# Kernel tuning notes

Measured on AMD Instinct MI355X. Metric: run time of the kernel, lower is better.

The kernel has to match this reference:

```python
import jax, jax.numpy as jnp
import numpy as np

C = 96        # dim
HEADS = 8     # FrameHistoryRouter heads (StateAlignBlock forces heads=1)
WS = 4        # window_size = 2*scale_patchsize
NFC = 1       # num_frames_tocache
TOPK = 5
LOCAL_N = 4


def conv(x, w, stride=1, pad=0, groups=1):
    return jax.lax.conv_general_dilated(
        x, w, (stride, stride), [(pad, pad), (pad, pad)],
        dimension_numbers=("NCHW", "OIHW", "NCHW"), feature_group_count=groups)


def l2norm(x, axis):
    n = jnp.linalg.norm(x, axis=axis, keepdims=True)
    return x / jnp.maximum(n, 1e-12)


def setup_inputs() -> dict:
    key = jax.random.key(0)
    ks = jax.random.split(key, 16)
    def rn(i, shp, s=0.02):
        return jax.random.normal(ks[i], shp, dtype=jnp.float32) * s
    return {
        "x": jax.random.normal(ks[0], (2, C, 256, 256), dtype=jnp.float32),
        "sab_qk_w": rn(1, (2 * C, C, 1, 1)),
        "sab_qk_dw": rn(2, (2 * C, 1, 3, 3)),
        "sab_v_w": rn(3, (C, C, 1, 1)),
        "sab_v_dw": rn(4, (C, 1, 3, 3)),
        "sab_k2_w": rn(5, (2 * C, C, 1, 1)),
        "sab_k2_dw": rn(6, (2 * C, 1, WS, WS)),
        "sab_q2_w": rn(7, (2 * C, C, 1, 1)),
        "sab_q2_dw": rn(8, (2 * C, 1, WS, WS)),
        "sab_proj_w": rn(9, (C, C, 1, 1)),
        "sab_temp": jnp.ones((1, 1, 1), jnp.float32),
        "fhr_qkv_w": rn(10, (3 * C, C, 1, 1)),
        "fhr_qkv_dw": rn(11, (3 * C, 1, 3, 3)),
        "fhr_proj_w": rn(12, (C, C, 1, 1)),
        "fhr_temp": jnp.ones((HEADS, 1, 1), jnp.float32),
    }


def _forward(x, sab_qk_w, sab_qk_dw, sab_v_w, sab_v_dw, sab_k2_w, sab_k2_dw,
             sab_q2_w, sab_q2_dw, sab_proj_w, sab_temp,
             fhr_qkv_w, fhr_qkv_dw, fhr_proj_w, fhr_temp):
    b, c, h, w = x.shape
    # ---------- StateAlignBlock (no cache: first frame) ----------
    qk = conv(conv(x, sab_qk_w), sab_qk_dw, pad=1, groups=2 * c)
    q, k = jnp.split(qk, 2, axis=1)
    v = conv(conv(x, sab_v_w), sab_v_dw, pad=1, groups=c)
    k = conv(conv(k, sab_k2_w), sab_k2_dw, stride=WS, pad=1, groups=2 * c)
    q = conv(conv(q, sab_q2_w), sab_q2_dw, stride=WS, pad=1, groups=2 * c)
    H, W = q.shape[2], q.shape[3]            # = h//WS, w//WS
    N = H * W
    # b (1 d) h w -> b 1 1 (h w) d   with d = 2c
    q = q.reshape(b, 2 * c, N).transpose(0, 2, 1)[:, None, None]
    k = k.reshape(b, 2 * c, N).transpose(0, 2, 1)[:, None, None]
    # v: b (1 d) (p1 h) (p2 w) -> b 1 1 (h w) (p1 p2 d), p1=p2=WS, d=c
    h2, w2 = h // WS, w // WS
    v = v.reshape(b, c, WS, h2, WS, w2).transpose(0, 3, 5, 2, 4, 1)
    v = v.reshape(b, 1, 1, h2 * w2, WS * WS * c)
    q = l2norm(q, -1)
    k = l2norm(k, -1)
    attn = jnp.einsum("bfgnd,bfgmd->bfgnm", q, k) * sab_temp  # [b,1,1,N,N]
    # zero_out_non_top_k (top-5 along last dim; threshold form, ties negligible)
    kth = jax.lax.top_k(attn, TOPK)[0][..., TOPK - 1:TOPK]
    topk_mask = (attn >= kth).astype(attn.dtype)
    # local attention mask: manhattan distance <= LOCAL_N on the HxW patch grid
    yy, xx = jnp.meshgrid(jnp.arange(H), jnp.arange(W), indexing="ij")
    coords = jnp.stack([yy.ravel(), xx.ravel()], axis=-1)          # [N,2]
    dist = jnp.abs(coords[:, None, :] - coords[None, :, :]).sum(-1)
    local = (dist <= LOCAL_N).astype(attn.dtype)                   # [N,N]
    attn = attn * topk_mask + attn * local                         # as in torch
    # clipped_softmax
    zero = attn == 0
    s = jax.nn.softmax(jnp.where(zero, -jnp.inf, attn), axis=-1)
    s = jnp.where(zero, 0.0, s)
    s = s / s.sum(-1, keepdims=True)
    out = jnp.einsum("bfgnm,bfgmd->bfgnd", s, v)  # [b,1,1,N, WS*WS*c]
    F = 1  # curr_num_frames (no cache)
    # b f 1 (h w) (p1 p2 d) -> (b f) d (p1 h) (p2 w)
    out = out.reshape(b * F, h2, w2, WS, WS, c).transpose(0, 5, 3, 1, 4, 2)
    out = out.reshape(b * F, c, h, w)
    out = conv(out, sab_proj_w)
    aligned = out.reshape(b, F, c, h, w)
    k_s = k[:, -NFC:]  # [b,1,1,N,2c]
    v_s = v[:, -NFC:]
    # ---------- FrameHistoryRouter on aligned current frame ----------
    x2 = aligned[:, -1]
    qkv = conv(conv(x2, fhr_qkv_w), fhr_qkv_dw, pad=1, groups=3 * c)
    q2, k2, v2 = jnp.split(qkv, 3, axis=1)
    hd = c // HEADS
    q2 = q2.reshape(b, HEADS, hd, h * w)
    k2 = k2.reshape(b, HEADS, hd, h * w)
    v2 = v2.reshape(b, HEADS, hd, h * w)
    q2 = l2norm(q2, -1)
    k2 = l2norm(k2, -1)
    a2 = jnp.einsum("bhcn,bhdn->bhcd", q2, k2) * fhr_temp  # [b,H,hd,hd]
    a2 = jax.nn.softmax(a2, axis=-1)
    o2 = jnp.einsum("bhcd,bhdn->bhcn", a2, v2).reshape(b, c, h, w)
    o2 = conv(o2, fhr_proj_w)
    keep = int(NFC * c / HEADS)  # = hd
    return o2, k_s, v_s, k2[:, :, -keep:, :], v2[:, :, -keep:, :]


def reference(x, sab_qk_w, sab_qk_dw, sab_v_w, sab_v_dw, sab_k2_w, sab_k2_dw,
              sab_q2_w, sab_q2_dw, sab_proj_w, sab_temp,
              fhr_qkv_w, fhr_qkv_dw, fhr_proj_w, fhr_temp):
    return _forward(x, sab_qk_w, sab_qk_dw, sab_v_w, sab_v_dw, sab_k2_w,
                    sab_k2_dw, sab_q2_w, sab_q2_dw, sab_proj_w, sab_temp,
                    fhr_qkv_w, fhr_qkv_dw, fhr_proj_w, fhr_temp)
```

## Files before the change

kernel.cpp:

```cpp
#include <hip/hip_runtime.h>
#include <hip/hip_bf16.h>
#include <math.h>

#define HW 65536L

typedef __attribute__((ext_vector_type(8))) short bf16x8;
typedef __attribute__((ext_vector_type(4))) float f32x4;

__device__ __forceinline__ int iabs_(int v) { return v < 0 ? -v : v; }

__device__ __forceinline__ void rtn_split(float f, unsigned short* h, unsigned short* l) {
  __hip_bfloat16 hb = __float2bfloat16(f);
  float hf = __bfloat162float(hb);
  __hip_bfloat16 lb = __float2bfloat16(f - hf);
  *h = *(unsigned short*)&hb;
  *l = *(unsigned short*)&lb;
}

__global__ __launch_bounds__(256) void wsplit(
    const float* __restrict__ qk, const float* __restrict__ v,
    const float* __restrict__ q2, const float* __restrict__ k2,
    unsigned short* __restrict__ whl)
{
  const int e = blockIdx.x*256 + threadIdx.x;
  if (e >= 64512) return;
  const int row = e / 96, col = e - row*96;
  float f;
  if      (row <  192) f = qk[e];
  else if (row <  288) f = v [(row-192)*96+col];
  else if (row <  480) f = q2[(row-288)*96+col];
  else                 f = k2[(row-480)*96+col];
  rtn_split(f, &whl[e], &whl[110592 + e]);
}

__global__ __launch_bounds__(256) void wcomp1(
    const float* __restrict__ fq, const float* __restrict__ pj,
    unsigned short* __restrict__ whl)
{
  const int e = blockIdx.x*256 + threadIdx.x;
  if (e >= 27648) return;
  const int row = e / 96, col = e - row*96;
  float s = 0.f;
  #pragma unroll 8
  for (int c = 0; c < 96; c++) s = fmaf(fq[row*96 + c], pj[c*96 + col], s);
  rtn_split(s, &whl[(768+row)*96 + col], &whl[110592 + (768+row)*96 + col]);
}

__global__ __launch_bounds__(256) void wcomp2(
    const float* __restrict__ fp, const float* __restrict__ a2s,
    unsigned short* __restrict__ w2)
{
  const int e = blockIdx.x*256 + threadIdx.x;
  const int b = blockIdx.y;
  if (e >= 9216) return;
  const int co = e / 96, dg = e - co*96;
  const int h = dg / 12, d = dg - h*12;
  const float* ab = a2s + (((long)b*8 + h)*12)*12 + d;
  const float* fpb = fp + co*96 + h*12;
  float s = 0.f;
  #pragma unroll
  for (int c = 0; c < 12; c++) s = fmaf(fpb[c], ab[c*12], s);
  rtn_split(s, &w2[(long)b*9216 + e], &w2[18432 + (long)b*9216 + e]);
}

#define BLDS 104
__global__ __launch_bounds__(256) void conv1x1_mfma(
    const float* __restrict__ in, long in_bstride,
    const unsigned short* __restrict__ whl_hi, const unsigned short* __restrict__ whl_lo,
    long wbstride, int wrow0,
    float* __restrict__ out, long out_bstride,
    float* __restrict__ out2, long out2_bstride,
    float* __restrict__ out3, long out3_bstride,
    int ms1, int ms2, int mtiles, int mode)
{
  __shared__ unsigned short bhs[128*BLDS];
  __shared__ unsigned short bls[128*BLDS];
  const int t = threadIdx.x;
  const int p0 = blockIdx.x * 128;
  const int b = blockIdx.y;
  if (mode == 0) {
    #pragma unroll
    for (int it = 0; it < 6; it++) {
      const int idx = it*256 + t;
      const int g8 = idx >> 7;
      const int pix = idx & 127;
      const float* src = in + (long)b*in_bstride + (long)(g8*8)*HW + p0 + pix;
      unsigned hh[8], ll[8];
      #pragma unroll
      for (int j = 0; j < 8; j++) {
        float f = src[(long)j*HW];
        unsigned u = __float_as_uint(f);
        hh[j] = u >> 16;
        float lof = f - __uint_as_float(u & 0xFFFF0000u);
        __hip_bfloat16 lb = __float2bfloat16(lof);
        ll[j] = *(unsigned short*)&lb;
      }
      uint4 hv, lv;
      hv.x = hh[0]|(hh[1]<<16); hv.y = hh[2]|(hh[3]<<16);
      hv.z = hh[4]|(hh[5]<<16); hv.w = hh[6]|(hh[7]<<16);
      lv.x = ll[0]|(ll[1]<<16); lv.y = ll[2]|(ll[3]<<16);
      lv.z = ll[4]|(ll[5]<<16); lv.w = ll[6]|(ll[7]<<16);
      *(uint4*)(bhs + pix*BLDS + g8*8) = hv;
      *(uint4*)(bls + pix*BLDS + g8*8) = lv;
    }
  } else {
    const int pp = t >> 1, half = (t & 1)*48;
    const int p = p0 + pp;
    const int py = p >> 8, px = p & 255;
    const float* src = in + (long)b*in_bstride
        + ((long)((py & 63)*64 + (px & 63))*16 + ((py >> 6)*4 + (px >> 6)))*96 + half;
    #pragma unroll
    for (int j4 = 0; j4 < 12; j4++) {
      float4 v4 = *(const float4*)&src[j4*4];
      float fv[4] = {v4.x, v4.y, v4.z, v4.w};
      unsigned hh[4], ll[4];
      #pragma unroll
      for (int u4 = 0; u4 < 4; u4++) {
        unsigned u = __float_as_uint(fv[u4]);
        hh[u4] = u >> 16;
        float lof = fv[u4] - __uint_as_float(u & 0xFFFF0000u);
        __hip_bfloat16 lb = __float2bfloat16(lof);
        ll[u4] = *(unsigned short*)&lb;
      }
      uint2 hv, lv;
      hv.x = hh[0] | (hh[1] << 16); hv.y = hh[2] | (hh[3] << 16);
      lv.x = ll[0] | (ll[1] << 16); lv.y = ll[2] | (ll[3] << 16);
      *(uint2*)(bhs + pp*BLDS + half + j4*4) = hv;
      *(uint2*)(bls + pp*BLDS + half + j4*4) = lv;
    }
  }
  __syncthreads();
  const int lane = t & 63, w = t >> 6;
  const int fr = lane & 15, fk = lane >> 4;
  bf16x8 Bh[2][3], Bl[2][3];
  #pragma unroll
  for (int nt = 0; nt < 2; nt++)
    #pragma unroll
    for (int kt = 0; kt < 3; kt++) {
      const int pix = w*32 + nt*16 + fr;
      Bh[nt][kt] = *(const bf16x8*)(bhs + pix*BLDS + kt*32 + fk*8);
      Bl[nt][kt] = *(const bf16x8*)(bls + pix*BLDS + kt*32 + fk*8);
    }
  const long wb = (long)b*wbstride;
  for (int m = 0; m < mtiles; m++) {
    const long wbase = wb + (long)(wrow0 + m*16 + fr)*96 + fk*8;
    bf16x8 Ah[3], Al[3];
    #pragma unroll
    for (int kt = 0; kt < 3; kt++) {
      Ah[kt] = *(const bf16x8*)(whl_hi + wbase + kt*32);
      Al[kt] = *(const bf16x8*)(whl_lo + wbase + kt*32);
    }
    f32x4 acc[2] = {};
    #pragma unroll
    for (int nt = 0; nt < 2; nt++)
      #pragma unroll
      for (int kt = 0; kt < 3; kt++) {
        acc[nt] = __builtin_amdgcn_mfma_f32_16x16x32_bf16(Ah[kt], Bh[nt][kt], acc[nt], 0, 0, 0);
        acc[nt] = __builtin_amdgcn_mfma_f32_16x16x32_bf16(Ah[kt], Bl[nt][kt], acc[nt], 0, 0, 0);
        acc[nt] = __builtin_amdgcn_mfma_f32_16x16x32_bf16(Al[kt], Bh[nt][kt], acc[nt], 0, 0, 0);
      }
    int mo; float* dst;
    if (m < ms1)      { mo = m;       dst = out  + (long)b*out_bstride; }
    else if (m < ms2) { mo = m - ms1; dst = out2 + (long)b*out2_bstride; }
    else              { mo = m - ms2; dst = out3 + (long)b*out3_bstride; }
    dst += p0 + w*32;
    #pragma unroll
    for (int nt = 0; nt < 2; nt++)
      #pragma unroll
      for (int r = 0; r < 4; r++)
        dst[(long)(mo*16 + fk*4 + r)*HW + nt*16 + fr] = acc[nt][r];
  }
}

__global__ __launch_bounds__(256) void dw3x3v(
    const float* __restrict__ in, int inCH, const float* __restrict__ w,
    float* __restrict__ out, int outCH)
{
  const int t = threadIdx.x;
  const int p4 = blockIdx.x * 256 + t;
  const int ch = blockIdx.y, b = blockIdx.z;
  const int y = p4 >> 6, x0 = (p4 & 63) << 2;
  const float* ip = in + ((long)b*inCH + ch) * HW;
  const float* wp = w + ch*9;
  float a0 = 0.f, a1 = 0.f, a2 = 0.f, a3 = 0.f;
  #pragma unroll
  for (int dy = -1; dy <= 1; dy++) {
    const int yy = y + dy;
    if (yy < 0 || yy > 255) continue;
    const float* rp = ip + yy*256;
    const float4 c = *(const float4*)&rp[x0];
    const float left  = (x0 > 0)   ? rp[x0-1] : 0.f;
    const float right = (x0 < 252) ? rp[x0+4] : 0.f;
    const float w0 = wp[(dy+1)*3+0], w1 = wp[(dy+1)*3+1], w2 = wp[(dy+1)*3+2];
    a0 = fmaf(left, w0, a0); a0 = fmaf(c.x, w1, a0); a0 = fmaf(c.y, w2, a0);
    a1 = fmaf(c.x,  w0, a1); a1 = fmaf(c.y, w1, a1); a1 = fmaf(c.z, w2, a1);
    a2 = fmaf(c.y,  w0, a2); a2 = fmaf(c.z, w1, a2); a2 = fmaf(c.w, w2, a2);
    a3 = fmaf(c.z,  w0, a3); a3 = fmaf(c.w, w1, a3); a3 = fmaf(right, w2, a3);
  }
  float4 o; o.x = a0; o.y = a1; o.z = a2; o.w = a3;
  *(float4*)&out[((long)b*outCH + ch)*HW + y*256 + x0] = o;
}

__global__ __launch_bounds__(256) void dw3x3_vs(
    const float* __restrict__ in, const float* __restrict__ w,
    float* __restrict__ vs)
{
  __shared__ float tile[96*65];
  const int t = threadIdx.x;
  const int gb = blockIdx.x;
  const int b = blockIdx.y;
  const int y = gb >> 2, xb = gb & 3;
  #pragma unroll
  for (int i = 0; i < 6; i++) {
    const int idx = i*256 + t;
    const int ci = idx >> 4, q = idx & 15;
    const int x0 = xb*64 + q*4;
    const float* ip = in + ((long)b*96 + ci) * HW;
    const float* wp = w + ci*9;
    float a0 = 0.f, a1 = 0.f, a2 = 0.f, a3 = 0.f;
    #pragma unroll
    for (int dy = -1; dy <= 1; dy++) {
      const int yy = y + dy;
      if (yy < 0 || yy > 255) continue;
      const float* rp = ip + yy*256;
      const float4 c = *(const float4*)&rp[x0];
      const float left  = (x0 > 0)   ? rp[x0-1] : 0.f;
      const float right = (x0 < 252) ? rp[x0+4] : 0.f;
      const float w0 = wp[(dy+1)*3+0], w1 = wp[(dy+1)*3+1], w2 = wp[(dy+1)*3+2];
      a0 = fmaf(left, w0, a0); a0 = fmaf(c.x, w1, a0); a0 = fmaf(c.y, w2, a0);
      a1 = fmaf(c.x,  w0, a1); a1 = fmaf(c.y, w1, a1); a1 = fmaf(c.z, w2, a1);
      a2 = fmaf(c.y,  w0, a2); a2 = fmaf(c.z, w1, a2); a2 = fmaf(c.w, w2, a2);
      a3 = fmaf(c.z,  w0, a3); a3 = fmaf(c.w, w1, a3); a3 = fmaf(right, w2, a3);
    }
    const int xl = q*4;
    tile[ci*65 + xl    ] = a0;
    tile[ci*65 + xl + 1] = a1;
    tile[ci*65 + xl + 2] = a2;
    tile[ci*65 + xl + 3] = a3;
  }
  __syncthreads();
  const int blk = (y >> 6)*4 + xb;
  float* obase = vs + ((long)b*4096 + (long)(y & 63)*64) * 1536 + blk*96;
  #pragma unroll
  for (int i = 0; i < 24; i++) {
    const int idx = i*256 + t;
    const int nl = idx / 96, ci = idx % 96;
    obase[(long)nl*1536 + ci] = tile[ci*65 + nl];
  }
}

__global__ __launch_bounds__(256) void dw4x4s4v(
    const float* __restrict__ in, const float* __restrict__ w,
    float* __restrict__ out)
{
  const int t = threadIdx.x;
  const int p = blockIdx.x*256 + t;
  const int ch = blockIdx.y, b = blockIdx.z;
  const int oy = p >> 4, qx = p & 15;
  const int x0 = qx*16;
  const float* ip = in + (long)(b*192 + ch) * HW;
  const float* wp = w + ch*16;
  float a0 = 0.f, a1 = 0.f, a2 = 0.f, a3 = 0.f;
  #pragma unroll
  for (int ty = 0; ty < 4; ty++) {
    const int iy = 4*oy + ty - 1;
    if (iy < 0 || iy > 255) continue;
    const float* rp = ip + iy*256;
    float r[17];
    r[0] = (x0 > 0) ? rp[x0-1] : 0.f;
    #pragma unroll
    for (int k = 0; k < 4; k++) {
      float4 v4 = *(const float4*)&rp[x0 + k*4];
      r[1+k*4+0]=v4.x; r[1+k*4+1]=v4.y; r[1+k*4+2]=v4.z; r[1+k*4+3]=v4.w;
    }
    const float w0=wp[ty*4+0], w1=wp[ty*4+1], w2=wp[ty*4+2], w3=wp[ty*4+3];
    a0=fmaf(r[ 0],w0,a0); a0=fmaf(r[ 1],w1,a0); a0=fmaf(r[ 2],w2,a0); a0=fmaf(r[ 3],w3,a0);
    a1=fmaf(r[ 4],w0,a1); a1=fmaf(r[ 5],w1,a1); a1=fmaf(r[ 6],w2,a1); a1=fmaf(r[ 7],w3,a1);
    a2=fmaf(r[ 8],w0,a2); a2=fmaf(r[ 9],w1,a2); a2=fmaf(r[10],w2,a2); a2=fmaf(r[11],w3,a2);
    a3=fmaf(r[12],w0,a3); a3=fmaf(r[13],w1,a3); a3=fmaf(r[14],w2,a3); a3=fmaf(r[15],w3,a3);
  }
  float4 o; o.x=a0; o.y=a1; o.z=a2; o.w=a3;
  *(float4*)&out[(long)(b*192 + ch)*4096 + oy*64 + qx*4] = o;
}

__global__ __launch_bounds__(256) void l2n192(
    const float* __restrict__ inA, float* __restrict__ outA,
    const float* __restrict__ inB, float* __restrict__ outB)
{
  const int t = threadIdx.x;
  const int wid = t >> 6, lane = t & 63;
  const int gw2 = blockIdx.x * 4 + wid;
  const int sel = gw2 >> 13;
  const int gw = gw2 & 8191;
  const int b = gw >> 12, n = gw & 4095;
  const float* ip = (sel ? inB : inA) + (long)b * 786432;
  float v0 = ip[(long)(lane      ) * 4096 + n];
  float v1 = ip[(long)(lane +  64) * 4096 + n];
  float v2 = ip[(long)(lane + 128) * 4096 + n];
  float ss = v0*v0 + v1*v1 + v2*v2;
  #pragma unroll
  for (int s = 1; s < 64; s <<= 1) ss += __shfl_xor(ss, s, 64);
  float nrm = fmaxf(sqrtf(ss), 1e-12f);
  float* op = (sel ? outB : outA) + ((long)b*4096 + n) * 192;
  op[lane      ] = v0 / nrm;
  op[lane +  64] = v1 / nrm;
  op[lane + 128] = v2 / nrm;
}

__global__ __launch_bounds__(256) void bf16split(
    const float* __restrict__ in, unsigned short* __restrict__ outp)
{
  const int i = blockIdx.x * 256 + threadIdx.x;
  const int n = i / 192, k = i % 192;
  float f = in[i];
  unsigned short h, l;
  rtn_split(f, &h, &l);
  outp[(long)n*384 + k]       = h;
  outp[(long)n*384 + 192 + k] = l;
}

#define LDSROW 40
__global__ __launch_bounds__(256) void attn_qk_mfma(
    const unsigned short* __restrict__ Qsp, const unsigned short* __restrict__ Ksp,
    float* __restrict__ attn, const float* __restrict__ tp)
{
  __shared__ unsigned short qs[256*LDSROW];
  __shared__ unsigned short ks[256*LDSROW];
  const int t = threadIdx.x;
  const int lane = t & 63, w = t >> 6;
  const int n0 = blockIdx.x * 128;
  const int m0 = blockIdx.y * 128;
  const int wr = (w >> 1) * 64, wc = (w & 1) * 64;
  f32x4 acc[4][4] = {};
  const int srow = t & 127;
  const int shl  = t >> 7;
  const unsigned short* qsrc = Qsp + (long)(n0 + srow) * 384 + shl * 192;
  const unsigned short* ksrc = Ksp + (long)(m0 + srow) * 384 + shl * 192;
  unsigned short* qdst = qs + (shl*128 + srow) * LDSROW;
  unsigned short* kdst = ks + (shl*128 + srow) * LDSROW;
  const int fr = lane & 15;
  const int fk = lane >> 4;
  for (int s = 0; s < 6; s++) {
    __syncthreads();
    #pragma unroll
    for (int j = 0; j < 4; j++) {
      *(bf16x8*)(qdst + j*8) = *(const bf16x8*)(qsrc + s*32 + j*8);
      *(bf16x8*)(kdst + j*8) = *(const bf16x8*)(ksrc + s*32 + j*8);
    }
    __syncthreads();
    bf16x8 ah[4], al[4], bh[4], bl[4];
    #pragma unroll
    for (int i = 0; i < 4; i++) {
      ah[i] = *(const bf16x8*)(qs + (      wr + i*16 + fr) * LDSROW + fk*8);
      al[i] = *(const bf16x8*)(qs + (128 + wr + i*16 + fr) * LDSROW + fk*8);
      bh[i] = *(const bf16x8*)(ks + (      wc + i*16 + fr) * LDSROW + fk*8);
      bl[i] = *(const bf16x8*)(ks + (128 + wc + i*16 + fr) * LDSROW + fk*8);
    }
    #pragma unroll
    for (int i = 0; i < 4; i++)
      #pragma unroll
      for (int j = 0; j < 4; j++) {
        acc[i][j] = __builtin_amdgcn_mfma_f32_16x16x32_bf16(ah[i], bh[j], acc[i][j], 0, 0, 0);
        acc[i][j] = __builtin_amdgcn_mfma_f32_16x16x32_bf16(ah[i], bl[j], acc[i][j], 0, 0, 0);
        acc[i][j] = __builtin_amdgcn_mfma_f32_16x16x32_bf16(al[i], bh[j], acc[i][j], 0, 0, 0);
      }
  }
  const float temp = tp[0];
  #pragma unroll
  for (int i = 0; i < 4; i++)
    #pragma unroll
    for (int j = 0; j < 4; j++)
      #pragma unroll
      for (int r = 0; r < 4; r++) {
        const int nn = n0 + wr + i*16 + (lane >> 4)*4 + r;
        const int mm = m0 + wc + j*16 + (lane & 15);
        attn[(long)nn*4096 + mm] = acc[i][j][r] * temp;
      }
}

#define CAP 128
__global__ __launch_bounds__(256) void attn_out_k(
    const float* __restrict__ attn, const float* __restrict__ vs,
    float* __restrict__ outr)
{
  __shared__ float row[4096];
  __shared__ float top5[256*5];
  __shared__ int   lm[CAP];
  __shared__ float lw[CAP];
  __shared__ float ses[CAP];
  __shared__ float redf[8];
  __shared__ int   wsum[4];
  const int t = threadIdx.x;
  const int n = blockIdx.x;
  const float* ar = attn + (long)n * 4096;
  #pragma unroll
  for (int k = 0; k < 16; k++) row[k*256 + t] = ar[k*256 + t];
  __syncthreads();
  float t0=-INFINITY,t1=-INFINITY,t2=-INFINITY,t3=-INFINITY,t4=-INFINITY;
  #pragma unroll
  for (int k = 0; k < 16; k++) {
    float v = row[k*256 + t];
    if (v > t4) {
      if (v > t0)      { t4=t3; t3=t2; t2=t1; t1=t0; t0=v; }
      else if (v > t1) { t4=t3; t3=t2; t2=t1; t1=v; }
      else if (v > t2) { t4=t3; t3=t2; t2=v; }
      else if (v > t3) { t4=t3; t3=v; }
      else             { t4=v; }
    }
  }
  top5[t*5+0]=t0; top5[t*5+1]=t1; top5[t*5+2]=t2; top5[t*5+3]=t3; top5[t*5+4]=t4;
  __syncthreads();
  for (int s = 128; s >= 1; s >>= 1) {
    if (t < s) {
      float* A = &top5[t*5];
      const float* B = &top5[(t+s)*5];
      float m[5]; int i = 0, j = 0;
      #pragma unroll
      for (int k = 0; k < 5; k++) {
        float av = A[i], bv = B[j];
        if (av >= bv) { m[k] = av; i++; } else { m[k] = bv; j++; }
      }
      #pragma unroll
      for (int k = 0; k < 5; k++) A[k] = m[k];
    }
    __syncthreads();
  }
  const float kth = top5[4];
  const int y = n >> 6, x = n & 63;
  int myc = 0;
  float wmax = -INFINITY;
  #pragma unroll
  for (int k = 0; k < 16; k++) {
    int m = k*256 + t;
    float a = row[m];
    int c = ((a >= kth) ? 1 : 0) +
            (((iabs_(y - (m >> 6)) + iabs_(x - (m & 63))) <= 4) ? 1 : 0);
    float wv = a * (float)c;
    if (wv != 0.0f) { myc++; wmax = fmaxf(wmax, wv); }
  }
  int inc = myc;
  #pragma unroll
  for (int s = 1; s < 64; s <<= 1) {
    int v = __shfl_up(inc, s, 64);
    if ((t & 63) >= s) inc += v;
  }
  if ((t & 63) == 63) wsum[t >> 6] = inc;
  __syncthreads();
  int pre = 0;
  #pragma unroll
  for (int wj = 0; wj < 4; wj++) pre += (wj < (t >> 6)) ? wsum[wj] : 0;
  const int base = pre + inc - myc;
  const int cnt = wsum[0] + wsum[1] + wsum[2] + wsum[3];
  {
    int idx = base;
    #pragma unroll
    for (int k = 0; k < 16; k++) {
      int m = k*256 + t;
      float a = row[m];
      int c = ((a >= kth) ? 1 : 0) +
              (((iabs_(y - (m >> 6)) + iabs_(x - (m & 63))) <= 4) ? 1 : 0);
      float wv = a * (float)c;
      if (wv != 0.0f && idx < CAP) { lm[idx] = m; lw[idx] = wv; idx++; }
    }
  }
  #pragma unroll
  for (int s = 1; s < 64; s <<= 1) wmax = fmaxf(wmax, __shfl_xor(wmax, s, 64));
  if ((t & 63) == 0) redf[t >> 6] = wmax;
  __syncthreads();
  const float gmax = fmaxf(fmaxf(redf[0], redf[1]), fmaxf(redf[2], redf[3]));
  __syncthreads();
  if (t < cnt && t < CAP) ses[t] = expf(lw[t] - gmax);
  __syncthreads();
  float ps = (t < cnt && t < CAP) ? ses[t] : 0.f;
  #pragma unroll
  for (int s = 1; s < 64; s <<= 1) ps += __shfl_xor(ps, s, 64);
  if ((t & 63) == 0) redf[4 + (t >> 6)] = ps;
  __syncthreads();
  const float S = redf[4] + redf[5] + redf[6] + redf[7];
  const float invS = 1.0f / S;
  float a0=0,a1=0,a2=0,a3=0,a4=0,a5=0;
  const int ecnt = (cnt < CAP) ? cnt : CAP;
  for (int e = 0; e < ecnt; e++) {
    float se = ses[e] * invS;
    const float* vr = vs + (long)lm[e] * 1536;
    a0 = fmaf(se, vr[        t], a0);
    a1 = fmaf(se, vr[ 256 + t], a1);
    a2 = fmaf(se, vr[ 512 + t], a2);
    a3 = fmaf(se, vr[ 768 + t], a3);
    a4 = fmaf(se, vr[1024 + t], a4);
    a5 = fmaf(se, vr[1280 + t], a5);
  }
  float* orow = outr + (long)n * 1536;
  orow[        t] = a0;
  orow[ 256 + t] = a1;
  orow[ 512 + t] = a2;
  orow[ 768 + t] = a3;
  orow[1024 + t] = a4;
  orow[1280 + t] = a5;
}

__global__ __launch_bounds__(1024) void l2n_sp(
    const float* __restrict__ in, float* __restrict__ out)
{
  const int ch = blockIdx.x, b = blockIdx.y, t = threadIdx.x;
  const float* ip = in + ((long)b*96 + ch) * HW;
  float ss = 0.f;
  for (int i = t; i < 65536; i += 1024) { float v = ip[i]; ss = fmaf(v, v, ss); }
  __shared__ float red[16];
  #pragma unroll
  for (int s = 1; s < 64; s <<= 1) ss += __shfl_xor(ss, s, 64);
  if ((t & 63) == 0) red[t >> 6] = ss;
  __syncthreads();
  if (t == 0) {
    float s2 = 0.f;
    for (int i = 0; i < 16; i++) s2 += red[i];
    red[0] = fmaxf(sqrtf(s2), 1e-12f);
  }
  __syncthreads();
  const float nrm = red[0];
  float* op = out + ((long)b*96 + ch) * HW;
  for (int i = t; i < 65536; i += 1024) op[i] = ip[i] / nrm;
}

#define A2_NCH 16
__global__ __launch_bounds__(256) void a2_part(
    const float* __restrict__ q2n, const float* __restrict__ k2n,
    float* __restrict__ part, float* __restrict__ qqpart)
{
  __shared__ float sh[24*260];
  const int t = threadIdx.x;
  const int ch = blockIdx.x, h = blockIdx.y, b = blockIdx.z;
  const long base = ((long)b*96 + h*12) * HW + ch*4096;
  const int c = t / 12, d = t - (t/12)*12;
  float acc = 0.f;
  float qq = 0.f;
  for (int sub = 0; sub < 16; sub++) {
    __syncthreads();
    #pragma unroll
    for (int j = 0; j < 6; j++) {
      const int v = j*256 + t;
      const int row = v >> 6;
      const int col4 = v & 63;
      const float* src = (row < 12)
        ? q2n + base + (long)row*HW + sub*256 + col4*4
        : k2n + base + (long)(row-12)*HW + sub*256 + col4*4;
      *(float4*)&sh[row*260 + col4*4] = *(const float4*)src;
    }
    __syncthreads();
    if (t < 144) {
      const float* qr = &sh[c*260];
      const float* kr = &sh[(12+d)*260];
      #pragma unroll
      for (int i4 = 0; i4 < 64; i4++) {
        float4 qv = *(const float4*)&qr[i4*4];
        float4 kv = *(const float4*)&kr[i4*4];
        acc = fmaf(qv.x, kv.x, acc);
        acc = fmaf(qv.y, kv.y, acc);
        acc = fmaf(qv.z, kv.z, acc);
        acc = fmaf(qv.w, kv.w, acc);
      }
    } else if (t < 156) {
      const float* qr = &sh[(t-144)*260];
      #pragma unroll
      for (int i4 = 0; i4 < 64; i4++) {
        float4 qv = *(const float4*)&qr[i4*4];
        qq = fmaf(qv.x, qv.x, qq);
        qq = fmaf(qv.y, qv.y, qq);
        qq = fmaf(qv.z, qv.z, qq);
        qq = fmaf(qv.w, qv.w, qq);
      }
    }
  }
  if (t < 144)
    part[(((long)b*8 + h)*A2_NCH + ch)*144 + t] = acc;
  else if (t < 156)
    qqpart[(((long)b*8 + h)*A2_NCH + ch)*12 + (t-144)] = qq;
}

__global__ __launch_bounds__(256) void a2_fin(
    const float* __restrict__ part, const float* __restrict__ qqpart,
    const float* __restrict__ temp, float* __restrict__ a2s)
{
  __shared__ float m[144];
  __shared__ float qn[12];
  const int t = threadIdx.x;
  const int h = blockIdx.x, b = blockIdx.y;
  if (t < 144) {
    float s = 0.f;
    const float* pp = part + (((long)b*8 + h)*A2_NCH)*144 + t;
    #pragma unroll
    for (int ch = 0; ch < A2_NCH; ch++) s += pp[ch*144];
    m[t] = s;
  } else if (t < 156) {
    float s = 0.f;
    const float* pp = qqpart + (((long)b*8 + h)*A2_NCH)*12 + (t-144);
    #pragma unroll
    for (int ch = 0; ch < A2_NCH; ch++) s += pp[ch*12];
    qn[t-144] = fmaxf(sqrtf(s), 1e-12f);
  }
  __syncthreads();
  if (t < 12) {
    const float tv = temp[h];
    const float scale = tv / qn[t];
    float mx = -INFINITY;
    float a[12];
    #pragma unroll
    for (int d = 0; d < 12; d++) { a[d] = m[t*12+d] * scale; mx = fmaxf(mx, a[d]); }
    float e[12], sum = 0.f;
    #pragma unroll
    for (int d = 0; d < 12; d++) { e[d] = expf(a[d]-mx); sum += e[d]; }
    float inv = 1.0f/sum;
    float* op = a2s + (((long)b*8 + h)*12 + t)*12;
    #pragma unroll
    for (int d = 0; d < 12; d++) op[d] = e[d]*inv;
  }
}

extern "C" void kernel_launch(void* const* d_in, const int* in_sizes, int n_in,
                              void* d_out, int out_size, void* d_ws, size_t ws_size,
                              hipStream_t stream) {
  const float* x        = (const float*)d_in[0];
  const float* qk_w     = (const float*)d_in[1];
  const float* qk_dw    = (const float*)d_in[2];
  const float* v_w      = (const float*)d_in[3];
  const float* v_dw     = (const float*)d_in[4];
  const float* k2_w     = (const float*)d_in[5];
  const float* k2_dw    = (const float*)d_in[6];
  const float* q2_w     = (const float*)d_in[7];
  const float* q2_dw    = (const float*)d_in[8];
  const float* proj_w   = (const float*)d_in[9];
  const float* sab_temp = (const float*)d_in[10];
  const float* fqkv_w   = (const float*)d_in[11];
  const float* fqkv_dw  = (const float*)d_in[12];
  const float* fproj_w  = (const float*)d_in[13];
  const float* fhr_temp = (const float*)d_in[14];
  float* out = (float*)d_out;
  float* ws  = (float*)d_ws;

  float* O2  = out;
  float* KS  = out + 12582912;
  float* VS  = out + 14155776;
  float* K2N = out + 26738688;
  float* V2  = out + 39321600;

  float* A0   = ws;
  float* A1   = ws + 25165824;
  float* QD   = ws + 50331648;
  float* KD   = ws + 51904512;
  float* QN   = ws + 53477376;
  float* A2S  = ws + 55050240;
  float* PART = ws + 55052544;
  unsigned short* QSP = (unsigned short*)(A0 + 16777216);
  unsigned short* KSP = (unsigned short*)(A0 + 16777216 + 786432);
  unsigned short* WHL = (unsigned short*)QN;
  float* P1  = ws;
  float* P2  = ws + 12582912;
  float* P3  = ws + 37748736;
  float* ALNQ = P2;
  float* QQP = QD;
  unsigned short* W2HL = (unsigned short*)PART;

  dim3 b256(256), b1024(1024);

  wsplit<<<dim3(252), b256, 0, stream>>>(qk_w, v_w, q2_w, k2_w, WHL);
  conv1x1_mfma<<<dim3(512,2), b256, 0, stream>>>(
      x, 96L*HW, WHL, WHL+110592, 0, 0,
      A0, 192L*HW, A1, 96L*HW, A1, 96L*HW, 12, 18, 18, 0);
  dw3x3_vs<<<dim3(1024,2), b256, 0, stream>>>(A1, v_dw, VS);
  dw3x3v<<<dim3(64,192,2), b256, 0, stream>>>(A0, 192, qk_dw, A1, 192);
  conv1x1_mfma<<<dim3(512,2), b256, 0, stream>>>(
      A1, 192L*HW, WHL, WHL+110592, 0, 288,
      A0, 192L*HW, A0, 192L*HW, A0, 192L*HW, 12, 12, 12, 0);
  dw4x4s4v<<<dim3(4,192,2), b256, 0, stream>>>(A0, q2_dw, QD);
  conv1x1_mfma<<<dim3(512,2), b256, 0, stream>>>(
      A1 + 96L*HW, 192L*HW, WHL, WHL+110592, 0, 480,
      A0, 192L*HW, A0, 192L*HW, A0, 192L*HW, 12, 12, 12, 0);
  dw4x4s4v<<<dim3(4,192,2), b256, 0, stream>>>(A0, k2_dw, KD);
  l2n192<<<dim3(4096), b256, 0, stream>>>(QD, QN, KD, KS);
  for (int b = 0; b < 2; b++) {
    bf16split<<<dim3(3072), b256, 0, stream>>>(QN + (long)b*786432, QSP);
    bf16split<<<dim3(3072), b256, 0, stream>>>(KS + (long)b*786432, KSP);
    attn_qk_mfma<<<dim3(32,32), b256, 0, stream>>>(QSP, KSP, A0, sab_temp);
    attn_out_k<<<dim3(4096), b256, 0, stream>>>(
        A0, VS + (long)b*6291456, A1 + (long)b*6291456);
  }
  wcomp1<<<dim3(108), b256, 0, stream>>>(fqkv_w, proj_w, WHL);
  conv1x1_mfma<<<dim3(512,2), b256, 0, stream>>>(
      A1, 6291456L, WHL, WHL+110592, 0, 768,
      P1, 96L*HW, P2, 96L*HW, P3, 96L*HW, 6, 12, 18, 1);
  dw3x3v<<<dim3(64,96,2), b256, 0, stream>>>(P2, 96, fqkv_dw +  864, K2N, 96);
  dw3x3v<<<dim3(64,96,2), b256, 0, stream>>>(P3, 96, fqkv_dw + 1728, V2,  96);
  dw3x3v<<<dim3(64,96,2), b256, 0, stream>>>(P1, 96, fqkv_dw,        ALNQ, 96);
  l2n_sp<<<dim3(96,2), b1024, 0, stream>>>(K2N, K2N);
  a2_part<<<dim3(A2_NCH,8,2), b256, 0, stream>>>(ALNQ, K2N, PART, QQP);
  a2_fin<<<dim3(8,2), b256, 0, stream>>>(PART, QQP, fhr_temp, A2S);
  wcomp2<<<dim3(36,2), b256, 0, stream>>>(fproj_w, A2S, W2HL);
  conv1x1_mfma<<<dim3(512,2), b256, 0, stream>>>(
      V2, 96L*HW, W2HL, W2HL+18432, 9216, 0,
      O2, 96L*HW, O2, 96L*HW, O2, 96L*HW, 6, 6, 6, 0);
}
```

Measured before the change: 831.3 us.

## Batch attention kernels across both images and keep attention rows in registers

Removes the per-batch host loop by giving the QK MFMA and attention-output kernels a batch grid dimension and making the bf16 split kernels cover both batches. Workspace buffers are rearranged so both batches' attention matrices and outputs coexist. attn_out_k now keeps each attention row in registers instead of LDS and caches the masked weights, which avoids recomputing them. It also permutes the row-to-block mapping, presumably to improve cache locality. The aim is fewer launches, more parallelism per launch, and less LDS traffic, at the cost of extra workspace memory and register pressure.

```diff
diff --git a/kernel.cpp b/kernel.cpp
--- a/kernel.cpp
+++ b/kernel.cpp
@@ -330,12 +330,16 @@
   const int lane = t & 63, w = t >> 6;
   const int n0 = blockIdx.x * 128;
   const int m0 = blockIdx.y * 128;
+  const int bb = blockIdx.z;
+  const unsigned short* Qb = Qsp + (long)bb*1572864;
+  const unsigned short* Kb = Ksp + (long)bb*1572864;
+  float* attb = attn + (long)bb*16777216;
   const int wr = (w >> 1) * 64, wc = (w & 1) * 64;
   f32x4 acc[4][4] = {};
   const int srow = t & 127;
   const int shl  = t >> 7;
-  const unsigned short* qsrc = Qsp + (long)(n0 + srow) * 384 + shl * 192;
-  const unsigned short* ksrc = Ksp + (long)(m0 + srow) * 384 + shl * 192;
+  const unsigned short* qsrc = Qb + (long)(n0 + srow) * 384 + shl * 192;
+  const unsigned short* ksrc = Kb + (long)(m0 + srow) * 384 + shl * 192;
   unsigned short* qdst = qs + (shl*128 + srow) * LDSROW;
   unsigned short* kdst = ks + (shl*128 + srow) * LDSROW;
   const int fr = lane & 15;
@@ -374,7 +378,7 @@
       for (int r = 0; r < 4; r++) {
         const int nn = n0 + wr + i*16 + (lane >> 4)*4 + r;
         const int mm = m0 + wc + j*16 + (lane & 15);
-        attn[(long)nn*4096 + mm] = acc[i][j][r] * temp;
+        attb[(long)nn*4096 + mm] = acc[i][j][r] * temp;
       }
 }
 
@@ -383,7 +387,6 @@
     const float* __restrict__ attn, const float* __restrict__ vs,
     float* __restrict__ outr)
 {
-  __shared__ float row[4096];
   __shared__ float top5[256*5];
   __shared__ int   lm[CAP];
   __shared__ float lw[CAP];
@@ -391,15 +394,17 @@
   __shared__ float redf[8];
   __shared__ int   wsum[4];
   const int t = threadIdx.x;
-  const int n = blockIdx.x;
-  const float* ar = attn + (long)n * 4096;
-  #pragma unroll
-  for (int k = 0; k < 16; k++) row[k*256 + t] = ar[k*256 + t];
-  __syncthreads();
+  const int bid = blockIdx.x;
+  const int n = ((bid & 7) << 9) | (bid >> 3);
+  const int bb = blockIdx.y;
+  const float* ar = attn + (long)bb*16777216 + (long)n * 4096;
+  const float* vsb = vs + (long)bb*6291456;
+  float av[16];
   float t0=-INFINITY,t1=-INFINITY,t2=-INFINITY,t3=-INFINITY,t4=-INFINITY;
   #pragma unroll
   for (int k = 0; k < 16; k++) {
-    float v = row[k*256 + t];
+    float v = ar[k*256 + t];
+    av[k] = v;
     if (v > t4) {
       if (v > t0)      { t4=t3; t3=t2; t2=t1; t1=t0; t0=v; }
       else if (v > t1) { t4=t3; t3=t2; t2=t1; t1=v; }
@@ -417,8 +422,8 @@
       float m[5]; int i = 0, j = 0;
       #pragma unroll
       for (int k = 0; k < 5; k++) {
-        float av = A[i], bv = B[j];
-        if (av >= bv) { m[k] = av; i++; } else { m[k] = bv; j++; }
+        float avv = A[i], bv = B[j];
+        if (avv >= bv) { m[k] = avv; i++; } else { m[k] = bv; j++; }
       }
       #pragma unroll
       for (int k = 0; k < 5; k++) A[k] = m[k];
@@ -429,13 +434,15 @@
   const int y = n >> 6, x = n & 63;
   int myc = 0;
   float wmax = -INFINITY;
+  float fv[16];
   #pragma unroll
   for (int k = 0; k < 16; k++) {
     int m = k*256 + t;
-    float a = row[m];
+    float a = av[k];
     int c = ((a >= kth) ? 1 : 0) +
             (((iabs_(y - (m >> 6)) + iabs_(x - (m & 63))) <= 4) ? 1 : 0);
     float wv = a * (float)c;
+    fv[k] = wv;
     if (wv != 0.0f) { myc++; wmax = fmaxf(wmax, wv); }
   }
   int inc = myc;
@@ -455,12 +462,8 @@
     int idx = base;
     #pragma unroll
     for (int k = 0; k < 16; k++) {
-      int m = k*256 + t;
-      float a = row[m];
-      int c = ((a >= kth) ? 1 : 0) +
-              (((iabs_(y - (m >> 6)) + iabs_(x - (m & 63))) <= 4) ? 1 : 0);
-      float wv = a * (float)c;
-      if (wv != 0.0f && idx < CAP) { lm[idx] = m; lw[idx] = wv; idx++; }
+      float wv = fv[k];
+      if (wv != 0.0f && idx < CAP) { lm[idx] = k*256 + t; lw[idx] = wv; idx++; }
     }
   }
   #pragma unroll
@@ -482,7 +485,7 @@
   const int ecnt = (cnt < CAP) ? cnt : CAP;
   for (int e = 0; e < ecnt; e++) {
     float se = ses[e] * invS;
-    const float* vr = vs + (long)lm[e] * 1536;
+    const float* vr = vsb + (long)lm[e] * 1536;
     a0 = fmaf(se, vr[        t], a0);
     a1 = fmaf(se, vr[ 256 + t], a1);
     a2 = fmaf(se, vr[ 512 + t], a2);
@@ -490,7 +493,7 @@
     a4 = fmaf(se, vr[1024 + t], a4);
     a5 = fmaf(se, vr[1280 + t], a5);
   }
-  float* orow = outr + (long)n * 1536;
+  float* orow = outr + (long)bb*6291456 + (long)n * 1536;
   orow[        t] = a0;
   orow[ 256 + t] = a1;
   orow[ 512 + t] = a2;
@@ -650,12 +653,14 @@
   float* QN   = ws + 53477376;
   float* A2S  = ws + 55050240;
   float* PART = ws + 55052544;
-  unsigned short* QSP = (unsigned short*)(A0 + 16777216);
-  unsigned short* KSP = (unsigned short*)(A0 + 16777216 + 786432);
   unsigned short* WHL = (unsigned short*)QN;
+  float* ATT  = ws;
+  unsigned short* QSP = (unsigned short*)(ws + 33554432);
+  unsigned short* KSP = (unsigned short*)(ws + 35127296);
+  float* AOUT = ws + 37748736;
   float* P1  = ws;
   float* P2  = ws + 12582912;
-  float* P3  = ws + 37748736;
+  float* P3  = ws + 25165824;
   float* ALNQ = P2;
   float* QQP = QD;
   unsigned short* W2HL = (unsigned short*)PART;
@@ -677,16 +682,13 @@
       A0, 192L*HW, A0, 192L*HW, A0, 192L*HW, 12, 12, 12, 0);
   dw4x4s4v<<<dim3(4,192,2), b256, 0, stream>>>(A0, k2_dw, KD);
   l2n192<<<dim3(4096), b256, 0, stream>>>(QD, QN, KD, KS);
-  for (int b = 0; b < 2; b++) {
-    bf16split<<<dim3(3072), b256, 0, stream>>>(QN + (long)b*786432, QSP);
-    bf16split<<<dim3(3072), b256, 0, stream>>>(KS + (long)b*786432, KSP);
-    attn_qk_mfma<<<dim3(32,32), b256, 0, stream>>>(QSP, KSP, A0, sab_temp);
-    attn_out_k<<<dim3(4096), b256, 0, stream>>>(
-        A0, VS + (long)b*6291456, A1 + (long)b*6291456);
-  }
+  bf16split<<<dim3(6144), b256, 0, stream>>>(QN, QSP);
+  bf16split<<<dim3(6144), b256, 0, stream>>>(KS, KSP);
+  attn_qk_mfma<<<dim3(32,32,2), b256, 0, stream>>>(QSP, KSP, ATT, sab_temp);
+  attn_out_k<<<dim3(4096,2), b256, 0, stream>>>(ATT, VS, AOUT);
   wcomp1<<<dim3(108), b256, 0, stream>>>(fqkv_w, proj_w, WHL);
   conv1x1_mfma<<<dim3(512,2), b256, 0, stream>>>(
-      A1, 6291456L, WHL, WHL+110592, 0, 768,
+      AOUT, 6291456L, WHL, WHL+110592, 0, 768,
       P1, 96L*HW, P2, 96L*HW, P3, 96L*HW, 6, 12, 18, 1);
   dw3x3v<<<dim3(64,96,2), b256, 0, stream>>>(P2, 96, fqkv_dw +  864, K2N, 96);
   dw3x3v<<<dim3(64,96,2), b256, 0, stream>>>(P3, 96, fqkv_dw + 1728, V2,  96);
```

New measurement: 805.8 us. 3.1% less time.
